# Kernel optimization log

Measured on AMD Instinct MI355X. Metric: run time of the kernel, lower is better.

## Reference

```python
import jax, jax.numpy as jnp
import numpy as np

# Tree / model dimensions
L = 1024          # number of leaves (batch rows of x)
F = 128           # num_features
H = 128           # num_dense_units
C = 10            # output_dim (num classes)
N = 2 * L - 1     # full binary tree node count
SPLICE = [0, F*H, F*H+H, F*H+H+H*H, F*H+2*H+H*H, F*H+2*H+H*H+H*C, F*H+2*H+H*H+H*C+C]
D = SPLICE[-1]    # 34314 = flattened sub-MLP weight count (layer_shape)
MIN_DIST = 1e-7


def setup_inputs() -> dict:
    key = jax.random.key(0)
    k1, k2, k3 = jax.random.split(key, 3)
    x = jax.random.normal(k1, (L, F), dtype=jnp.float32)
    # per-node AdditionLayer weight vectors (trainable deltas)
    W = jax.random.normal(k2, (N, D), dtype=jnp.float32) * 0.02
    heights = jax.random.uniform(k3, (N,), dtype=jnp.float32)
    p = (np.arange(N) - 1) // 2
    p[0] = 0  # root self-parent; root is excluded from the mut-distance term
    parent = jnp.asarray(p, dtype=jnp.int32)
    leaf_idx = jnp.arange(L - 1, N, dtype=jnp.int32)  # leaves in traversal order
    return {"x": x, "W": W, "heights": heights, "parent": parent, "leaf_idx": leaf_idx}


def reference(x, W, heights, parent, leaf_idx):
    n = W.shape[0]
    depth = int(np.log2(n + 1))
    # Effective weights per node = sum of AdditionLayer deltas along root->node path.
    # Level-by-level parent gather (parents at level d-1 are already accumulated).
    eff = W
    for d in range(1, depth):
        s, e = 2 ** d - 1, 2 ** (d + 1) - 1
        eff = eff.at[s:e].add(eff[parent[s:e]])

    # delta_tensor: root uses squared diff vs zero input (= sum(W_root^2));
    # every other node: curr - input = W_node, so sum|W_node| / mut_distance.
    mut = jnp.maximum(jnp.abs(heights - heights[parent]), MIN_DIST)  # [n]
    l1 = jnp.sum(jnp.abs(W), axis=1)                                 # [n]
    delta = jnp.sum(W[0] ** 2) + jnp.sum(l1[1:] / mut[1:])
    delta = jnp.reshape(delta, (1,))

    # Leaf sub-MLP: splice each leaf's effective weight vector into kernels/biases
    wl = eff[leaf_idx]                                  # [L, D]
    Lf = wl.shape[0]
    W0 = wl[:, SPLICE[0]:SPLICE[1]].reshape(Lf, F, H)
    b0 = wl[:, SPLICE[1]:SPLICE[2]]
    W1 = wl[:, SPLICE[2]:SPLICE[3]].reshape(Lf, H, H)
    b1 = wl[:, SPLICE[3]:SPLICE[4]]
    W2 = wl[:, SPLICE[4]:SPLICE[5]].reshape(Lf, H, C)
    b2 = wl[:, SPLICE[5]:SPLICE[6]]
    h = jax.nn.relu(jnp.einsum('lf,lfh->lh', x, W0) + b0)
    h = jax.nn.relu(jnp.einsum('lh,lhk->lk', h, W1) + b1)
    out = jax.nn.softmax(jnp.einsum('lh,lhc->lc', h, W2) + b2, axis=-1)
    return (out, delta)
```

## Files before the change

### kernel.cpp

```cpp
#include <hip/hip_runtime.h>

#define LN 1024
#define FF 128
#define HH 128
#define CC 10
#define DD 34314
#define DD2 17157
#define CHK 2145
#define OFF_W0 0
#define OFF_B0 16384
#define OFF_W1 16512
#define OFF_B1 32896
#define OFF_W2 33024
#define OFF_B2 34304

__global__ void init_delta(float* delta) { *delta = 0.f; }

__device__ __forceinline__ float invmut(const float* h, int node, int par) {
    return 1.f / fmaxf(fabsf(h[node] - h[par]), 1e-7f);
}

__global__ __launch_bounds__(1024) void eff5_kernel(const float* __restrict__ W,
                                                    const float* __restrict__ heights,
                                                    float* __restrict__ eff,
                                                    float* __restrict__ delta_out) {
    const int bid = blockIdx.x;
    const int n5  = bid >> 3;
    const int ck  = bid & 7;
    const int tid = threadIdx.x, lane = tid & 63, wv = tid >> 6;

    int p[6];
    p[0] = 31 + n5;
#pragma unroll
    for (int k = 1; k < 6; ++k) p[k] = (p[k - 1] - 1) >> 1;

    const float2* S[6];
#pragma unroll
    for (int k = 0; k < 6; ++k) S[k] = reinterpret_cast<const float2*>(W + (size_t)p[k] * DD);
    float2* E = reinterpret_cast<float2*>(eff + (size_t)n5 * DD);

    float wgt[6];
#pragma unroll
    for (int k = 0; k < 5; ++k)
        wgt[k] = ((n5 & ((1 << k) - 1)) == 0) ? invmut(heights, p[k], p[k + 1]) : 0.f;
    wgt[5] = 0.f;
    const float sqm = (n5 == 0) ? 1.f : 0.f;

    float dacc = 0.f, sacc = 0.f;
    const int lo = ck * CHK;
    const int hi = min(lo + CHK, DD2);
#pragma unroll 1
    for (int i = lo + tid; i < hi; i += 1024) {
        float ex = 0.f, ey = 0.f;
#pragma unroll
        for (int k = 0; k < 6; ++k) {
            const float2 w = S[k][i];
            ex += w.x; ey += w.y;
            dacc += (fabsf(w.x) + fabsf(w.y)) * wgt[k];
            if (k == 5) sacc += w.x * w.x + w.y * w.y;
        }
        E[i] = make_float2(ex, ey);
    }

    __shared__ float red[16];
    float v = dacc + sacc * sqm;
    for (int o = 32; o > 0; o >>= 1) v += __shfl_down(v, o);
    if (lane == 0) red[wv] = v;
    __syncthreads();
    if (tid == 0) {
        float s = 0.f;
#pragma unroll
        for (int w = 0; w < 16; ++w) s += red[w];
        atomicAdd(delta_out, s);
    }
}

__global__ __launch_bounds__(1024, 4)
__attribute__((amdgpu_waves_per_eu(4, 4)))
void fused_kernel(const float* __restrict__ W,
                  const float* __restrict__ eff,
                  const float* __restrict__ x,
                  const float* __restrict__ heights,
                  float* __restrict__ out,
                  float* __restrict__ delta_out) {
    const int bid  = blockIdx.x;
    const int m    = ((bid & 7) << 5) | (bid >> 3);
    const int tid  = threadIdx.x;
    const int lane = tid & 63;
    const int wv   = tid >> 6;
    const int j2   = lane;

    const int l8 = 255 + m;
    const int l7 = (l8 - 1) >> 1;
    const int l6 = (l7 - 1) >> 1;
    const int l5 = (l6 - 1) >> 1;

    const float* RE = eff + (size_t)(m >> 3) * DD;
    const float* RP[3];
    RP[0] = W + (size_t)l8 * DD;
    RP[1] = W + (size_t)l7 * DD;
    RP[2] = W + (size_t)l6 * DD;
    const int n9a = 511 + 2 * m, n9b = n9a + 1;
    const float* RA[2];
    RA[0] = W + (size_t)n9a * DD;
    RA[1] = W + (size_t)n9b * DD;
    const float* RB[4];
#pragma unroll
    for (int q = 0; q < 4; ++q) RB[q] = W + (size_t)(1023 + 4 * m + q) * DD;

    float wgtP[3];
    wgtP[0] = invmut(heights, l8, l7);
    wgtP[1] = ((m & 1) == 0) ? invmut(heights, l7, l6) : 0.f;
    wgtP[2] = ((m & 3) == 0) ? invmut(heights, l6, l5) : 0.f;
    float wgtA[2];
    wgtA[0] = invmut(heights, n9a, l8);
    wgtA[1] = invmut(heights, n9b, l8);
    float wgtB[4];
#pragma unroll
    for (int q = 0; q < 4; ++q)
        wgtB[q] = invmut(heights, 1023 + 4 * m + q, (q < 2) ? n9a : n9b);

    __shared__ float ins[4][HH];
    __shared__ float part[4][16][HH];
    __shared__ float lgts[4][CC];
    __shared__ float red[16];

    if (tid < 512) { const int q = tid >> 7, t = tid & 127; ins[q][t] = x[(4 * m + q) * FF + t]; }
    if (tid < 4 * CC) ((float*)lgts)[tid] = 0.f;

    float dacc = 0.f;
    __syncthreads();

#pragma unroll
    for (int layer = 0; layer < 2; ++layer) {
        const int offW = layer ? OFF_W1 : OFF_W0;
        const int offB = layer ? OFF_B1 : OFF_B0;
        const float2* SE = reinterpret_cast<const float2*>(RE + offW);
        const float2* SP[3];
#pragma unroll
        for (int r = 0; r < 3; ++r) SP[r] = reinterpret_cast<const float2*>(RP[r] + offW);
        const float2* SA[2];
#pragma unroll
        for (int r = 0; r < 2; ++r) SA[r] = reinterpret_cast<const float2*>(RA[r] + offW);
        const float2* SB[4];
#pragma unroll
        for (int r = 0; r < 4; ++r) SB[r] = reinterpret_cast<const float2*>(RB[r] + offW);

        float yx[4], yy[4];
#pragma unroll
        for (int q = 0; q < 4; ++q) { yx[q] = 0.f; yy[q] = 0.f; }

#pragma unroll 2
        for (int i = 0; i < 8; ++i) {
            const int f   = (wv << 3) + i;
            const int off = (f << 6) + j2;
            const float2 we = SE[off];
            float ex = we.x, ey = we.y;
#pragma unroll
            for (int k = 0; k < 3; ++k) {
                const float2 w = SP[k][off];
                ex += w.x; ey += w.y;
                dacc += (fabsf(w.x) + fabsf(w.y)) * wgtP[k];
            }
            const float2 wa0 = SA[0][off];
            const float2 wa1 = SA[1][off];
            dacc += (fabsf(wa0.x) + fabsf(wa0.y)) * wgtA[0];
            dacc += (fabsf(wa1.x) + fabsf(wa1.y)) * wgtA[1];
#pragma unroll
            for (int q = 0; q < 4; ++q) {
                const float2 wb = SB[q][off];
                dacc += (fabsf(wb.x) + fabsf(wb.y)) * wgtB[q];
                const float2 wa = (q < 2) ? wa0 : wa1;
                const float xv = ins[q][f];
                yx[q] += xv * (ex + wa.x + wb.x);
                yy[q] += xv * (ey + wa.y + wb.y);
            }
        }
#pragma unroll
        for (int q = 0; q < 4; ++q)
            *reinterpret_cast<float2*>(&part[q][wv][2 * j2]) = make_float2(yx[q], yy[q]);
        __syncthreads();

        if (tid < 512) {
            const int q = tid >> 7, col = tid & 127;
            const float p0 = RP[0][offB + col];
            const float p1 = RP[1][offB + col];
            const float p2 = RP[2][offB + col];
            float eb = RE[offB + col] + p0 + p1 + p2;
            if (q == 0)
                dacc += fabsf(p0) * wgtP[0] + fabsf(p1) * wgtP[1] + fabsf(p2) * wgtP[2];
            const float a0 = RA[0][offB + col];
            const float a1 = RA[1][offB + col];
            if (q == 0) dacc += fabsf(a0) * wgtA[0];
            if (q == 2) dacc += fabsf(a1) * wgtA[1];
            const float bq = RB[q][offB + col];
            dacc += fabsf(bq) * wgtB[q];
            float s = eb + ((q < 2) ? a0 : a1) + bq;
#pragma unroll
            for (int w = 0; w < 16; ++w) s += part[q][w][col];
            ins[q][col] = fmaxf(s, 0.f);
        }
        __syncthreads();
    }

    {
        const float2* SE = reinterpret_cast<const float2*>(RE + OFF_W2);
        const float2* SP[3];
#pragma unroll
        for (int r = 0; r < 3; ++r) SP[r] = reinterpret_cast<const float2*>(RP[r] + OFF_W2);
        const float2* SA[2];
#pragma unroll
        for (int r = 0; r < 2; ++r) SA[r] = reinterpret_cast<const float2*>(RA[r] + OFF_W2);
        const float2* SB[4];
#pragma unroll
        for (int r = 0; r < 4; ++r) SB[r] = reinterpret_cast<const float2*>(RB[r] + OFF_W2);
        if (tid < 640) {
            const int h  = tid / 5;
            const int c0 = (tid - 5 * h) * 2;
            const float2 we = SE[tid];
            float ex = we.x, ey = we.y;
#pragma unroll
            for (int k = 0; k < 3; ++k) {
                const float2 w = SP[k][tid];
                ex += w.x; ey += w.y;
                dacc += (fabsf(w.x) + fabsf(w.y)) * wgtP[k];
            }
            const float2 wa0 = SA[0][tid];
            const float2 wa1 = SA[1][tid];
            dacc += (fabsf(wa0.x) + fabsf(wa0.y)) * wgtA[0];
            dacc += (fabsf(wa1.x) + fabsf(wa1.y)) * wgtA[1];
#pragma unroll
            for (int q = 0; q < 4; ++q) {
                const float2 wb = SB[q][tid];
                dacc += (fabsf(wb.x) + fabsf(wb.y)) * wgtB[q];
                const float2 wa = (q < 2) ? wa0 : wa1;
                const float hv = ins[q][h];
                atomicAdd(&lgts[q][c0],     hv * (ex + wa.x + wb.x));
                atomicAdd(&lgts[q][c0 + 1], hv * (ey + wa.y + wb.y));
            }
        }
        __syncthreads();
        if (tid < CC) {
            const float p0 = RP[0][OFF_B2 + tid];
            const float p1 = RP[1][OFF_B2 + tid];
            const float p2 = RP[2][OFF_B2 + tid];
            float eb = RE[OFF_B2 + tid] + p0 + p1 + p2;
            dacc += fabsf(p0) * wgtP[0] + fabsf(p1) * wgtP[1] + fabsf(p2) * wgtP[2];
            const float a0 = RA[0][OFF_B2 + tid];
            const float a1 = RA[1][OFF_B2 + tid];
            dacc += fabsf(a0) * wgtA[0] + fabsf(a1) * wgtA[1];
#pragma unroll
            for (int q = 0; q < 4; ++q) {
                const float bq = RB[q][OFF_B2 + tid];
                dacc += fabsf(bq) * wgtB[q];
                lgts[q][tid] += eb + ((q < 2) ? a0 : a1) + bq;
            }
        }
        __syncthreads();
    }

    if (tid < 4) {
        const int q = tid;
        float mx = lgts[q][0];
#pragma unroll
        for (int c = 1; c < CC; ++c) mx = fmaxf(mx, lgts[q][c]);
        float e[CC], s = 0.f;
#pragma unroll
        for (int c = 0; c < CC; ++c) { e[c] = expf(lgts[q][c] - mx); s += e[c]; }
        const float inv = 1.f / s;
#pragma unroll
        for (int c = 0; c < CC; ++c) out[(4 * m + q) * CC + c] = e[c] * inv;
    }

    float v = dacc;
    for (int o = 32; o > 0; o >>= 1) v += __shfl_down(v, o);
    if (lane == 0) red[wv] = v;
    __syncthreads();
    if (tid == 0) {
        float s = 0.f;
#pragma unroll
        for (int w = 0; w < 16; ++w) s += red[w];
        atomicAdd(delta_out, s);
    }
}

extern "C" void kernel_launch(void* const* d_in, const int* in_sizes, int n_in,
                              void* d_out, int out_size, void* d_ws, size_t ws_size,
                              hipStream_t stream) {
    const float* x       = (const float*)d_in[0];
    const float* W       = (const float*)d_in[1];
    const float* heights = (const float*)d_in[2];

    float* out   = (float*)d_out;
    float* delta = (float*)d_out + LN * CC;
    float* eff   = (float*)d_ws;

    init_delta<<<1, 1, 0, stream>>>(delta);
    eff5_kernel<<<256, 1024, 0, stream>>>(W, heights, eff, delta);
    fused_kernel<<<256, 1024, 0, stream>>>(W, eff, x, heights, out, delta);
}
```

Baseline: 83.37 us.

## Split fused MLP kernel into per-layer kernels with column-split blocks

Replaces the single fused kernel (256 blocks, each handling 4 leaves through all three layers) with two per-layer kernels that split each layer's output columns across 2 blocks (512 blocks), plus a separate head kernel. Intermediate activations are written to and read back from workspace. The aim is more parallelism and occupancy for the dominant weight-streaming layers. The cost is two extra kernel launches, global round-trips for the hidden activations, and redundant re-reading of the bias and x vectors per half.

```diff
diff --git a/kernel.cpp b/kernel.cpp
--- a/kernel.cpp
+++ b/kernel.cpp
@@ -75,133 +75,159 @@
     }
 }
 
-__global__ __launch_bounds__(1024, 4)
-__attribute__((amdgpu_waves_per_eu(4, 4)))
-void fused_kernel(const float* __restrict__ W,
-                  const float* __restrict__ eff,
-                  const float* __restrict__ x,
-                  const float* __restrict__ heights,
-                  float* __restrict__ out,
-                  float* __restrict__ delta_out) {
-    const int bid  = blockIdx.x;
-    const int m    = ((bid & 7) << 5) | (bid >> 3);
-    const int tid  = threadIdx.x;
-    const int lane = tid & 63;
-    const int wv   = tid >> 6;
-    const int j2   = lane;
-
-    const int l8 = 255 + m;
-    const int l7 = (l8 - 1) >> 1;
-    const int l6 = (l7 - 1) >> 1;
-    const int l5 = (l6 - 1) >> 1;
-
-    const float* RE = eff + (size_t)(m >> 3) * DD;
-    const float* RP[3];
-    RP[0] = W + (size_t)l8 * DD;
-    RP[1] = W + (size_t)l7 * DD;
-    RP[2] = W + (size_t)l6 * DD;
-    const int n9a = 511 + 2 * m, n9b = n9a + 1;
-    const float* RA[2];
-    RA[0] = W + (size_t)n9a * DD;
-    RA[1] = W + (size_t)n9b * DD;
-    const float* RB[4];
-#pragma unroll
-    for (int q = 0; q < 4; ++q) RB[q] = W + (size_t)(1023 + 4 * m + q) * DD;
-
-    float wgtP[3];
-    wgtP[0] = invmut(heights, l8, l7);
-    wgtP[1] = ((m & 1) == 0) ? invmut(heights, l7, l6) : 0.f;
-    wgtP[2] = ((m & 3) == 0) ? invmut(heights, l6, l5) : 0.f;
-    float wgtA[2];
-    wgtA[0] = invmut(heights, n9a, l8);
-    wgtA[1] = invmut(heights, n9b, l8);
-    float wgtB[4];
+#define SETUP_STREAMS()                                                               \
+    const int l8 = 255 + m;                                                           \
+    const int l7 = (l8 - 1) >> 1;                                                     \
+    const int l6 = (l7 - 1) >> 1;                                                     \
+    const int l5 = (l6 - 1) >> 1;                                                     \
+    const float* RE = eff + (size_t)(m >> 3) * DD;                                    \
+    const float* RP[3];                                                               \
+    RP[0] = W + (size_t)l8 * DD;                                                      \
+    RP[1] = W + (size_t)l7 * DD;                                                      \
+    RP[2] = W + (size_t)l6 * DD;                                                      \
+    const int n9a = 511 + 2 * m, n9b = n9a + 1;                                       \
+    const float* RA[2];                                                               \
+    RA[0] = W + (size_t)n9a * DD;                                                     \
+    RA[1] = W + (size_t)n9b * DD;                                                     \
+    const float* RB[4];                                                               \
+    _Pragma("unroll")                                                                 \
+    for (int q = 0; q < 4; ++q) RB[q] = W + (size_t)(1023 + 4 * m + q) * DD;          \
+    float wgtP[3];                                                                    \
+    wgtP[0] = invmut(heights, l8, l7);                                                \
+    wgtP[1] = ((m & 1) == 0) ? invmut(heights, l7, l6) : 0.f;                         \
+    wgtP[2] = ((m & 3) == 0) ? invmut(heights, l6, l5) : 0.f;                         \
+    float wgtA[2];                                                                    \
+    wgtA[0] = invmut(heights, n9a, l8);                                               \
+    wgtA[1] = invmut(heights, n9b, l8);                                               \
+    float wgtB[4];                                                                    \
+    _Pragma("unroll")                                                                 \
+    for (int q = 0; q < 4; ++q)                                                       \
+        wgtB[q] = invmut(heights, 1023 + 4 * m + q, (q < 2) ? n9a : n9b);
+
+template <int OFFW, int OFFB>
+__global__ __launch_bounds__(1024, 8) void layer_split(const float* __restrict__ W,
+                                                       const float* __restrict__ eff,
+                                                       const float* __restrict__ invec,
+                                                       const float* __restrict__ heights,
+                                                       float* __restrict__ outvec,
+                                                       float* __restrict__ delta_out) {
+    const int bid = blockIdx.x;
+    const int u   = ((bid & 7) << 6) | (bid >> 3);
+    const int m   = u >> 1;
+    const int ch  = u & 1;
+    const int tid = threadIdx.x, lane = tid & 63, wv = tid >> 6;
+    const int fs  = tid >> 5;
+    const int cp  = tid & 31;
+
+    SETUP_STREAMS();
+
+    __shared__ float ins[4][FF];
+    __shared__ float part[4][32][64];
+    __shared__ float red[16];
+
+    if (tid < 512) { const int q = tid >> 7, t = tid & 127; ins[q][t] = invec[(4 * m + q) * FF + t]; }
+
+    float dacc = 0.f;
+    __syncthreads();
+
+    const float2* SE = reinterpret_cast<const float2*>(RE + OFFW);
+    const float2* SP[3];
+#pragma unroll
+    for (int r = 0; r < 3; ++r) SP[r] = reinterpret_cast<const float2*>(RP[r] + OFFW);
+    const float2* SA[2];
+#pragma unroll
+    for (int r = 0; r < 2; ++r) SA[r] = reinterpret_cast<const float2*>(RA[r] + OFFW);
+    const float2* SB[4];
+#pragma unroll
+    for (int r = 0; r < 4; ++r) SB[r] = reinterpret_cast<const float2*>(RB[r] + OFFW);
+
+    float yx[4] = {0.f, 0.f, 0.f, 0.f}, yy[4] = {0.f, 0.f, 0.f, 0.f};
+
+#pragma unroll 2
+    for (int it = 0; it < 4; ++it) {
+        const int f   = it * 32 + fs;
+        const int off = (f << 6) + (ch << 5) + cp;
+        const float2 we = SE[off];
+        float ex = we.x, ey = we.y;
+#pragma unroll
+        for (int k = 0; k < 3; ++k) {
+            const float2 w = SP[k][off];
+            ex += w.x; ey += w.y;
+            dacc += (fabsf(w.x) + fabsf(w.y)) * wgtP[k];
+        }
+        const float2 wa0 = SA[0][off];
+        const float2 wa1 = SA[1][off];
+        dacc += (fabsf(wa0.x) + fabsf(wa0.y)) * wgtA[0];
+        dacc += (fabsf(wa1.x) + fabsf(wa1.y)) * wgtA[1];
+#pragma unroll
+        for (int q = 0; q < 4; ++q) {
+            const float2 wb = SB[q][off];
+            dacc += (fabsf(wb.x) + fabsf(wb.y)) * wgtB[q];
+            const float2 wa = (q < 2) ? wa0 : wa1;
+            const float xv = ins[q][f];
+            yx[q] += xv * (ex + wa.x + wb.x);
+            yy[q] += xv * (ey + wa.y + wb.y);
+        }
+    }
 #pragma unroll
     for (int q = 0; q < 4; ++q)
-        wgtB[q] = invmut(heights, 1023 + 4 * m + q, (q < 2) ? n9a : n9b);
+        *reinterpret_cast<float2*>(&part[q][fs][2 * cp]) = make_float2(yx[q], yy[q]);
+    __syncthreads();
+
+    if (tid < 256) {
+        const int q = tid >> 6, col = tid & 63;
+        const int gcol = ch * 64 + col;
+        const float p0 = RP[0][OFFB + gcol];
+        const float p1 = RP[1][OFFB + gcol];
+        const float p2 = RP[2][OFFB + gcol];
+        float eb = RE[OFFB + gcol] + p0 + p1 + p2;
+        if (q == 0)
+            dacc += fabsf(p0) * wgtP[0] + fabsf(p1) * wgtP[1] + fabsf(p2) * wgtP[2];
+        const float a0 = RA[0][OFFB + gcol];
+        const float a1 = RA[1][OFFB + gcol];
+        if (q == 0) dacc += fabsf(a0) * wgtA[0];
+        if (q == 2) dacc += fabsf(a1) * wgtA[1];
+        const float bq = RB[q][OFFB + gcol];
+        dacc += fabsf(bq) * wgtB[q];
+        float s = eb + ((q < 2) ? a0 : a1) + bq;
+#pragma unroll
+        for (int g = 0; g < 32; ++g) s += part[q][g][col];
+        outvec[(4 * m + q) * HH + gcol] = fmaxf(s, 0.f);
+    }
+
+    float v = dacc;
+    for (int o = 32; o > 0; o >>= 1) v += __shfl_down(v, o);
+    if (lane == 0) red[wv] = v;
+    __syncthreads();
+    if (tid == 0) {
+        float s = 0.f;
+#pragma unroll
+        for (int w = 0; w < 16; ++w) s += red[w];
+        atomicAdd(delta_out, s);
+    }
+}
+
+__global__ __launch_bounds__(1024, 4) void head_kernel(const float* __restrict__ W,
+                                                       const float* __restrict__ eff,
+                                                       const float* __restrict__ ws_h1,
+                                                       const float* __restrict__ heights,
+                                                       float* __restrict__ out,
+                                                       float* __restrict__ delta_out) {
+    const int bid = blockIdx.x;
+    const int m   = ((bid & 7) << 5) | (bid >> 3);
+    const int tid = threadIdx.x, lane = tid & 63, wv = tid >> 6;
+
+    SETUP_STREAMS();
 
     __shared__ float ins[4][HH];
-    __shared__ float part[4][16][HH];
     __shared__ float lgts[4][CC];
     __shared__ float red[16];
 
-    if (tid < 512) { const int q = tid >> 7, t = tid & 127; ins[q][t] = x[(4 * m + q) * FF + t]; }
+    if (tid < 512) { const int q = tid >> 7, t = tid & 127; ins[q][t] = ws_h1[(4 * m + q) * HH + t]; }
     if (tid < 4 * CC) ((float*)lgts)[tid] = 0.f;
 
     float dacc = 0.f;
     __syncthreads();
-
-#pragma unroll
-    for (int layer = 0; layer < 2; ++layer) {
-        const int offW = layer ? OFF_W1 : OFF_W0;
-        const int offB = layer ? OFF_B1 : OFF_B0;
-        const float2* SE = reinterpret_cast<const float2*>(RE + offW);
-        const float2* SP[3];
-#pragma unroll
-        for (int r = 0; r < 3; ++r) SP[r] = reinterpret_cast<const float2*>(RP[r] + offW);
-        const float2* SA[2];
-#pragma unroll
-        for (int r = 0; r < 2; ++r) SA[r] = reinterpret_cast<const float2*>(RA[r] + offW);
-        const float2* SB[4];
-#pragma unroll
-        for (int r = 0; r < 4; ++r) SB[r] = reinterpret_cast<const float2*>(RB[r] + offW);
-
-        float yx[4], yy[4];
-#pragma unroll
-        for (int q = 0; q < 4; ++q) { yx[q] = 0.f; yy[q] = 0.f; }
-
-#pragma unroll 2
-        for (int i = 0; i < 8; ++i) {
-            const int f   = (wv << 3) + i;
-            const int off = (f << 6) + j2;
-            const float2 we = SE[off];
-            float ex = we.x, ey = we.y;
-#pragma unroll
-            for (int k = 0; k < 3; ++k) {
-                const float2 w = SP[k][off];
-                ex += w.x; ey += w.y;
-                dacc += (fabsf(w.x) + fabsf(w.y)) * wgtP[k];
-            }
-            const float2 wa0 = SA[0][off];
-            const float2 wa1 = SA[1][off];
-            dacc += (fabsf(wa0.x) + fabsf(wa0.y)) * wgtA[0];
-            dacc += (fabsf(wa1.x) + fabsf(wa1.y)) * wgtA[1];
-#pragma unroll
-            for (int q = 0; q < 4; ++q) {
-                const float2 wb = SB[q][off];
-                dacc += (fabsf(wb.x) + fabsf(wb.y)) * wgtB[q];
-                const float2 wa = (q < 2) ? wa0 : wa1;
-                const float xv = ins[q][f];
-                yx[q] += xv * (ex + wa.x + wb.x);
-                yy[q] += xv * (ey + wa.y + wb.y);
-            }
-        }
-#pragma unroll
-        for (int q = 0; q < 4; ++q)
-            *reinterpret_cast<float2*>(&part[q][wv][2 * j2]) = make_float2(yx[q], yy[q]);
-        __syncthreads();
-
-        if (tid < 512) {
-            const int q = tid >> 7, col = tid & 127;
-            const float p0 = RP[0][offB + col];
-            const float p1 = RP[1][offB + col];
-            const float p2 = RP[2][offB + col];
-            float eb = RE[offB + col] + p0 + p1 + p2;
-            if (q == 0)
-                dacc += fabsf(p0) * wgtP[0] + fabsf(p1) * wgtP[1] + fabsf(p2) * wgtP[2];
-            const float a0 = RA[0][offB + col];
-            const float a1 = RA[1][offB + col];
-            if (q == 0) dacc += fabsf(a0) * wgtA[0];
-            if (q == 2) dacc += fabsf(a1) * wgtA[1];
-            const float bq = RB[q][offB + col];
-            dacc += fabsf(bq) * wgtB[q];
-            float s = eb + ((q < 2) ? a0 : a1) + bq;
-#pragma unroll
-            for (int w = 0; w < 16; ++w) s += part[q][w][col];
-            ins[q][col] = fmaxf(s, 0.f);
-        }
-        __syncthreads();
-    }
 
     {
         const float2* SE = reinterpret_cast<const float2*>(RE + OFF_W2);
@@ -294,8 +320,12 @@
     float* out   = (float*)d_out;
     float* delta = (float*)d_out + LN * CC;
     float* eff   = (float*)d_ws;
+    float* ws_h0 = (float*)d_ws + 32 * DD;
+    float* ws_h1 = ws_h0 + LN * HH;
 
     init_delta<<<1, 1, 0, stream>>>(delta);
     eff5_kernel<<<256, 1024, 0, stream>>>(W, heights, eff, delta);
-    fused_kernel<<<256, 1024, 0, stream>>>(W, eff, x, heights, out, delta);
-}
+    layer_split<OFF_W0, OFF_B0><<<512, 1024, 0, stream>>>(W, eff, x, heights, ws_h0, delta);
+    layer_split<OFF_W1, OFF_B1><<<512, 1024, 0, stream>>>(W, eff, ws_h0, heights, ws_h1, delta);
+    head_kernel<<<256, 1024, 0, stream>>>(W, eff, ws_h1, heights, out, delta);
+}
```

Measured after the change: 106.5 us. +27.7%, slower.
